# Performance work log

Hardware: AMD Instinct MI355X
Metric: run time of the kernel (lower is better)

## Reference

```python
import jax, jax.numpy as jnp
import numpy as np

D_MODEL = 2048
N_HEADS = 32
N_KV_HEADS = 8
ROPE_BASE = 10000.0


def setup_inputs() -> dict:
    key = jax.random.key(0)
    ks = jax.random.split(key, 5)
    b, s, d = 2, 2048, D_MODEL
    hd = d // N_HEADS
    scale = 0.02
    return {
        "x": jax.random.normal(ks[0], (b, s, d), jnp.float32),
        "wq": jax.random.normal(ks[1], (N_HEADS * hd, d), jnp.float32) * scale,
        "wk": jax.random.normal(ks[2], (N_KV_HEADS * hd, d), jnp.float32) * scale,
        "wv": jax.random.normal(ks[3], (N_KV_HEADS * hd, d), jnp.float32) * scale,
        "wo": jax.random.normal(ks[4], (d, N_HEADS * hd), jnp.float32) * scale,
    }


def _rope_cos_sin(seq_len, head_dim):
    # theta_j = base^(-2j/d); freqs[i, j] = i * theta_j; repeat-interleave x2 on last dim
    theta = 1.0 / (ROPE_BASE ** (jnp.arange(0, head_dim, 2, dtype=jnp.float32) / head_dim))
    freqs = jnp.arange(seq_len, dtype=jnp.float32)[:, None] * theta[None, :]  # [S, hd/2]
    cos = jnp.repeat(jnp.cos(freqs), 2, axis=-1)[None, :, None, :]  # [1, S, 1, hd]
    sin = jnp.repeat(jnp.sin(freqs), 2, axis=-1)[None, :, None, :]
    return cos, sin


def _rotate(t):
    # interleaved rotate-half: (x0, x1, x2, x3, ...) -> (-x1, x0, -x3, x2, ...)
    t1 = t[..., ::2]
    t2 = t[..., 1::2]
    return jnp.stack([-t2, t1], axis=-1).reshape(t.shape)


def reference(x, wq, wk, wv, wo):
    b, s, d = x.shape
    hd = d // N_HEADS
    n_rep = N_HEADS // N_KV_HEADS

    q = (x @ wq.T).reshape(b, s, N_HEADS, hd)       # [b, s, H, hd]
    k = (x @ wk.T).reshape(b, s, N_KV_HEADS, hd)    # [b, s, G, hd]
    v = (x @ wv.T).reshape(b, s, N_KV_HEADS, hd)

    cos, sin = _rope_cos_sin(s, hd)
    q = q * cos + _rotate(q) * sin
    k = k * cos + _rotate(k) * sin

    # GQA without physical KV replication: group query heads by shared KV head.
    # repeat_interleave(n_rep, dim=2) maps kv head g -> query heads [g*n_rep, (g+1)*n_rep)
    qg = q.reshape(b, s, N_KV_HEADS, n_rep, hd)
    scale = 1.0 / jnp.sqrt(jnp.asarray(hd, q.dtype))
    scores = jnp.einsum('bqgrd,bkgd->bgrqk', qg, k) * scale  # [b, G, rep, Sq, Sk]

    causal = jnp.tril(jnp.ones((s, s), dtype=bool))
    scores = jnp.where(causal[None, None, None], scores, jnp.asarray(-jnp.inf, scores.dtype))
    attn = jax.nn.softmax(scores, axis=-1)

    out = jnp.einsum('bgrqk,bkgd->bqgrd', attn, v).reshape(b, s, N_HEADS * hd)
    return out @ wo.T
```

## Files before the change

### kernel.cpp

```cpp
#include <hip/hip_runtime.h>

typedef unsigned short u16;
typedef __attribute__((ext_vector_type(8))) short bf16x8;
typedef __attribute__((ext_vector_type(4))) float f32x4;

#define LOG2E 1.44269504088896340736f

__device__ inline u16 f2b(float f) {
    unsigned int u = __builtin_bit_cast(unsigned int, f);
    unsigned int r = u + 0x7fffu + ((u >> 16) & 1u);
    return (u16)(r >> 16);
}
__device__ inline float b2f(u16 h) {
    unsigned int u = ((unsigned int)h) << 16;
    return __builtin_bit_cast(float, u);
}

#define GLOAD_LDS16(g, l) \
    __builtin_amdgcn_global_load_lds( \
        (const __attribute__((address_space(1))) unsigned int*)(g), \
        (__attribute__((address_space(3))) unsigned int*)(l), 16, 0, 0)

__global__ __launch_bounds__(256) void cast_all(
    const float* __restrict__ x, const float* __restrict__ wq,
    const float* __restrict__ wk, const float* __restrict__ wv,
    const float* __restrict__ wo, u16* __restrict__ xb,
    u16* __restrict__ wqkvb, u16* __restrict__ wob) {
    long i = ((long)blockIdx.x * 256 + threadIdx.x) * 8;
    const float* s;
    u16* d;
    if (i < 8388608)       { s = x  + i;              d = xb + i; }
    else if (i < 12582912) { s = wq + (i - 8388608);  d = wqkvb + (i - 8388608); }
    else if (i < 13631488) { s = wk + (i - 12582912); d = wqkvb + 4194304 + (i - 12582912); }
    else if (i < 14680064) { s = wv + (i - 13631488); d = wqkvb + 5242880 + (i - 13631488); }
    else                   { s = wo + (i - 14680064); d = wob + (i - 14680064); }
    float4 v0 = *(const float4*)s;
    float4 v1 = *(const float4*)(s + 4);
    ushort4 o0 = make_ushort4(f2b(v0.x), f2b(v0.y), f2b(v0.z), f2b(v0.w));
    ushort4 o1 = make_ushort4(f2b(v1.x), f2b(v1.y), f2b(v1.z), f2b(v1.w));
    *(ushort4*)d = o0;
    *(ushort4*)(d + 4) = o1;
}

__global__ __launch_bounds__(256) void rope_vtrans(
    u16* __restrict__ qkv, u16* __restrict__ VT, float qscale) {
    const int S = 2048, RS = 3072;
    int tid = threadIdx.x;
    if (blockIdx.x < 5120) {
        int idx = blockIdx.x * 256 + tid;
        int row = idx / 320;
        int rem = idx - row * 320;
        int head = rem >> 3, chunk = rem & 7;
        int pos = row & 2047;
        int coloff;
        float scale;
        if (head < 32) { coloff = head * 64;               scale = qscale; }
        else           { coloff = 2048 + (head - 32) * 64; scale = 1.0f; }
        u16* p = qkv + (size_t)row * RS + coloff + chunk * 8;
        bf16x8 v = *(bf16x8*)p;
        float t0 = exp2f((float)(chunk * 4) * -0.41524101186092f);
        const float tc[4] = {1.0f, 0.74989420933246f, 0.56234132519035f, 0.42169650342858f};
        float fpos = (float)pos;
        #pragma unroll
        for (int i = 0; i < 4; i++) {
            float f = fpos * (t0 * tc[i]);
            float rev = f * 0.15915494309189535f;
            rev = rev - floorf(rev);
            float sn = __builtin_amdgcn_sinf(rev);
            float cs = __builtin_amdgcn_cosf(rev);
            float e0 = b2f((u16)v[2 * i]), e1 = b2f((u16)v[2 * i + 1]);
            v[2 * i]     = (short)f2b((e0 * cs - e1 * sn) * scale);
            v[2 * i + 1] = (short)f2b((e1 * cs + e0 * sn) * scale);
        }
        *(bf16x8*)p = v;
    } else {
        int bid = blockIdx.x - 5120;
        int st = bid & 31, g = (bid >> 5) & 7, b = bid >> 8;
        __shared__ u16 T[64 * 72];
        for (int c = tid; c < 512; c += 256) {
            int sr = c >> 3, dc = (c & 7) * 8;
            *(bf16x8*)&T[sr * 72 + dc] =
                *(const bf16x8*)(qkv + ((size_t)b * S + st * 64 + sr) * RS + 2560 + g * 64 + dc);
        }
        __syncthreads();
        for (int c = tid; c < 512; c += 256) {
            int d = c >> 3, sc = (c & 7) * 8;
            bf16x8 o;
            #pragma unroll
            for (int j = 0; j < 8; j++) o[j] = (short)T[(sc + j) * 72 + d];
            *(bf16x8*)(VT + ((size_t)((b * 8 + g) * 64 + d)) * S + st * 64 + sc) = o;
        }
    }
}

__global__ __launch_bounds__(256) void gemm_bt128(
    const u16* __restrict__ A, const u16* __restrict__ B, void* __restrict__ Cv,
    int M, int N, int K, int c_is_f32) {
    __shared__ u16 As[128 * 32];
    __shared__ u16 Bs[128 * 32];
    const int tid = threadIdx.x;
    const int lane = tid & 63, wave = tid >> 6;
    const int ln = lane & 15, quad = lane >> 4;
    const int wm = wave >> 1, wn = wave & 1;
    const int m0 = blockIdx.y * 128, n0 = blockIdx.x * 128;

    const int srow = wave * 16 + (lane >> 2);
    const int skc = (lane & 3) * 8;
    const u16* Ag = A + (size_t)(m0 + srow) * K + skc;
    const u16* Bg = B + (size_t)(n0 + srow) * K + skc;

    f32x4 acc[4][4] = {};
    for (int k0 = 0; k0 < K; k0 += 32) {
        #pragma unroll
        for (int t = 0; t < 2; t++) {
            GLOAD_LDS16(Ag + (size_t)t * 64 * K + k0, As + t * 2048 + wave * 512);
            GLOAD_LDS16(Bg + (size_t)t * 64 * K + k0, Bs + t * 2048 + wave * 512);
        }
        __syncthreads();

        bf16x8 af[4], bfr[4];
        #pragma unroll
        for (int i = 0; i < 4; i++) {
            af[i]  = *(const bf16x8*)&As[(wm * 64 + i * 16 + ln) * 32 + quad * 8];
            bfr[i] = *(const bf16x8*)&Bs[(wn * 64 + i * 16 + ln) * 32 + quad * 8];
        }
        #pragma unroll
        for (int mi = 0; mi < 4; mi++)
            #pragma unroll
            for (int nt = 0; nt < 4; nt++)
                acc[mi][nt] = __builtin_amdgcn_mfma_f32_16x16x32_bf16(
                    af[mi], bfr[nt], acc[mi][nt], 0, 0, 0);
        __syncthreads();
    }

    #pragma unroll
    for (int mi = 0; mi < 4; mi++)
        #pragma unroll
        for (int nt = 0; nt < 4; nt++)
            #pragma unroll
            for (int r = 0; r < 4; r++) {
                int row = m0 + wm * 64 + mi * 16 + quad * 4 + r;
                int col = n0 + wn * 64 + nt * 16 + ln;
                float v = acc[mi][nt][r];
                if (c_is_f32) ((float*)Cv)[(size_t)row * N + col] = v;
                else          ((u16*)Cv)[(size_t)row * N + col] = f2b(v);
            }
}

__global__ __launch_bounds__(256) void attn_kernel(
    const u16* __restrict__ QKV, const u16* __restrict__ VT, u16* __restrict__ O) {
    const int S = 2048, RS = 3072, DO = 2048;
    const int b = blockIdx.z, h = blockIdx.y, p = blockIdx.x;
    const int g = h >> 2;
    const int qtl = p, qth = (S / 64 - 1) - p;
    const int tid = threadIdx.x;
    const int lane = tid & 63, wave = tid >> 6;
    const int ln = lane & 15, quad = lane >> 4;

    __shared__ u16 Ks[64 * 72];
    __shared__ u16 Psh[64 * 68];
    __shared__ u16 Psl[64 * 68];

    const u16* Qb = QKV + (size_t)b * S * RS + h * 64 + quad * 8;
    bf16x8 aqh0 = *(const bf16x8*)(Qb + (size_t)(qth * 64 + wave * 16 + ln) * RS);
    bf16x8 aqh1 = *(const bf16x8*)(Qb + (size_t)(qth * 64 + wave * 16 + ln) * RS + 32);
    bf16x8 aql0 = *(const bf16x8*)(Qb + (size_t)(qtl * 64 + wave * 16 + ln) * RS);
    bf16x8 aql1 = *(const bf16x8*)(Qb + (size_t)(qtl * 64 + wave * 16 + ln) * RS + 32);

    const u16* Kb = QKV + (size_t)b * S * RS + 2048 + g * 64;
    const u16* VTb = VT + (size_t)(b * 8 + g) * 64 * S;

    const bf16x8 vones = {0x3F80, 0x3F80, 0x3F80, 0x3F80, 0x3F80, 0x3F80, 0x3F80, 0x3F80};

    f32x4 acch[5] = {}, accl[5] = {};

    const int r0 = tid >> 3;
    const int dc0 = (tid & 7) * 8;
    bf16x8 kreg0, kreg1;
    auto loadK = [&](int kt) {
        kreg0 = *(const bf16x8*)(Kb + (size_t)(kt * 64 + r0) * RS + dc0);
        kreg1 = *(const bf16x8*)(Kb + (size_t)(kt * 64 + r0 + 32) * RS + dc0);
    };

    auto body = [&](int kt, bool DUAL, bool MH, bool ML) {
        __syncthreads();
        *(bf16x8*)&Ks[r0 * 72 + dc0] = kreg0;
        *(bf16x8*)&Ks[(r0 + 32) * 72 + dc0] = kreg1;
        __syncthreads();
        if (kt < qth) loadK(kt + 1);

        bf16x8 vr[2][4];
        #pragma unroll
        for (int kk = 0; kk < 2; kk++)
            #pragma unroll
            for (int nt = 0; nt < 4; nt++)
                vr[kk][nt] = *(const bf16x8*)(VTb + (size_t)(nt * 16 + ln) * S
                                              + kt * 64 + kk * 32 + quad * 8);

        f32x4 sh[4] = {}, sl[4] = {};
        __builtin_amdgcn_s_setprio(1);
        #pragma unroll
        for (int nt = 0; nt < 4; nt++) {
            bf16x8 bk0 = *(const bf16x8*)&Ks[(nt * 16 + ln) * 72 + quad * 8];
            bf16x8 bk1 = *(const bf16x8*)&Ks[(nt * 16 + ln) * 72 + 32 + quad * 8];
            sh[nt] = __builtin_amdgcn_mfma_f32_16x16x32_bf16(aqh0, bk0, sh[nt], 0, 0, 0);
            sh[nt] = __builtin_amdgcn_mfma_f32_16x16x32_bf16(aqh1, bk1, sh[nt], 0, 0, 0);
            if (DUAL) {
                sl[nt] = __builtin_amdgcn_mfma_f32_16x16x32_bf16(aql0, bk0, sl[nt], 0, 0, 0);
                sl[nt] = __builtin_amdgcn_mfma_f32_16x16x32_bf16(aql1, bk1, sl[nt], 0, 0, 0);
            }
        }
        __builtin_amdgcn_s_setprio(0);

        if (MH) {
            #pragma unroll
            for (int nt = 0; nt < 4; nt++)
                #pragma unroll
                for (int r = 0; r < 4; r++)
                    if (nt * 16 + ln > wave * 16 + quad * 4 + r) sh[nt][r] = -INFINITY;
        }
        #pragma unroll
        for (int nt = 0; nt < 4; nt++)
            #pragma unroll
            for (int r = 0; r < 4; r++) {
                float pv = exp2f(sh[nt][r]);
                Psh[(wave * 16 + quad * 4 + r) * 68 + nt * 16 + ln] =
                    (u16)(__builtin_bit_cast(unsigned int, pv) >> 16);
            }
        if (DUAL) {
            if (ML) {
                #pragma unroll
                for (int nt = 0; nt < 4; nt++)
                    #pragma unroll
                    for (int r = 0; r < 4; r++)
                        if (nt * 16 + ln > wave * 16 + quad * 4 + r) sl[nt][r] = -INFINITY;
            }
            #pragma unroll
            for (int nt = 0; nt < 4; nt++)
                #pragma unroll
                for (int r = 0; r < 4; r++) {
                    float pv = exp2f(sl[nt][r]);
                    Psl[(wave * 16 + quad * 4 + r) * 68 + nt * 16 + ln] =
                        (u16)(__builtin_bit_cast(unsigned int, pv) >> 16);
                }
        }

        __builtin_amdgcn_s_setprio(1);
        #pragma unroll
        for (int kk = 0; kk < 2; kk++) {
            bf16x8 aph = *(const bf16x8*)&Psh[(wave * 16 + ln) * 68 + kk * 32 + quad * 8];
            #pragma unroll
            for (int nt = 0; nt < 4; nt++)
                acch[nt] = __builtin_amdgcn_mfma_f32_16x16x32_bf16(aph, vr[kk][nt], acch[nt], 0, 0, 0);
            acch[4] = __builtin_amdgcn_mfma_f32_16x16x32_bf16(aph, vones, acch[4], 0, 0, 0);
            if (DUAL) {
                bf16x8 apl = *(const bf16x8*)&Psl[(wave * 16 + ln) * 68 + kk * 32 + quad * 8];
                #pragma unroll
                for (int nt = 0; nt < 4; nt++)
                    accl[nt] = __builtin_amdgcn_mfma_f32_16x16x32_bf16(apl, vr[kk][nt], accl[nt], 0, 0, 0);
                accl[4] = __builtin_amdgcn_mfma_f32_16x16x32_bf16(apl, vones, accl[4], 0, 0, 0);
            }
        }
        __builtin_amdgcn_s_setprio(0);
    };

    loadK(0);
    for (int kt = 0; kt < qtl; kt++) body(kt, true, false, false);
    body(qtl, true, false, true);
    for (int kt = qtl + 1; kt < qth; kt++) body(kt, false, false, false);
    body(qth, false, true, false);

    u16* Ob = O + (size_t)b * S * DO + h * 64;
    #pragma unroll
    for (int r = 0; r < 4; r++) {
        float invh = 1.0f / acch[4][r];
        float invl = 1.0f / accl[4][r];
        int qh = qth * 64 + wave * 16 + quad * 4 + r;
        int ql = qtl * 64 + wave * 16 + quad * 4 + r;
        #pragma unroll
        for (int nt = 0; nt < 4; nt++) {
            Ob[(size_t)qh * DO + nt * 16 + ln] = f2b(acch[nt][r] * invh);
            Ob[(size_t)ql * DO + nt * 16 + ln] = f2b(accl[nt][r] * invl);
        }
    }
}

extern "C" void kernel_launch(void* const* d_in, const int* in_sizes, int n_in,
                              void* d_out, int out_size, void* d_ws, size_t ws_size,
                              hipStream_t stream) {
    const float* x  = (const float*)d_in[0];
    const float* wq = (const float*)d_in[1];
    const float* wk = (const float*)d_in[2];
    const float* wv = (const float*)d_in[3];
    const float* wo = (const float*)d_in[4];

    const int B = 2, S = 2048, D = 2048, H = 32, KVH = 8;
    const int M = B * S;
    const int NQKV = 3072;

    char* ws = (char*)d_ws;
    size_t off = 0;
    auto alloc = [&](size_t bytes) {
        void* p = ws + off;
        off += (bytes + 255) & ~(size_t)255;
        return p;
    };
    u16* xb    = (u16*)alloc((size_t)M * D * 2);
    u16* wqkvb = (u16*)alloc((size_t)NQKV * D * 2);
    u16* wob   = (u16*)alloc((size_t)D * D * 2);
    u16* QKV   = (u16*)alloc((size_t)M * NQKV * 2);
    u16* AO = xb;
    u16* VT = wqkvb;

    cast_all<<<dim3(9216), 256, 0, stream>>>(x, wq, wk, wv, wo, xb, wqkvb, wob);

    gemm_bt128<<<dim3(NQKV / 128, M / 128), 256, 0, stream>>>(xb, wqkvb, QKV, M, NQKV, D, 0);

    const float sscale = 0.125f * LOG2E;
    rope_vtrans<<<dim3(5632), 256, 0, stream>>>(QKV, VT, sscale);

    attn_kernel<<<dim3(S / 128, H, B), 256, 0, stream>>>(QKV, VT, AO);

    gemm_bt128<<<dim3(D / 128, M / 128), 256, 0, stream>>>(AO, wob, d_out, M, D, D, 1);
}
```

Baseline: 377.3 us.

## Double-buffer K tiles and prefetch V in attention; swizzle GEMM workgroups

Attention now keeps two LDS K tiles, loads K two tiles ahead and V one tile ahead in registers. This replaces the two barriers per iteration with a single one at the end of the body, so global load latency can overlap compute. The GEMM remaps workgroup IDs in chunks of eight, likely to improve L2 locality across XCDs. The cost is more LDS and more registers in attention, which could lower occupancy.

```diff
diff --git a/kernel.cpp b/kernel.cpp
--- a/kernel.cpp
+++ b/kernel.cpp
@@ -102,7 +102,13 @@
     const int lane = tid & 63, wave = tid >> 6;
     const int ln = lane & 15, quad = lane >> 4;
     const int wm = wave >> 1, wn = wave & 1;
-    const int m0 = blockIdx.y * 128, n0 = blockIdx.x * 128;
+
+    const int gx = gridDim.x;
+    const int nwg = gx * gridDim.y;
+    const int bid = blockIdx.y * gx + blockIdx.x;
+    const int cpx = nwg >> 3;
+    const int swz = (bid & 7) * cpx + (bid >> 3);
+    const int m0 = (swz / gx) * 128, n0 = (swz % gx) * 128;
 
     const int srow = wave * 16 + (lane >> 2);
     const int skc = (lane & 3) * 8;
@@ -157,7 +163,7 @@
     const int lane = tid & 63, wave = tid >> 6;
     const int ln = lane & 15, quad = lane >> 4;
 
-    __shared__ u16 Ks[64 * 72];
+    __shared__ u16 Ks[2][64 * 72];
     __shared__ u16 Psh[64 * 68];
     __shared__ u16 Psl[64 * 68];
 
@@ -177,32 +183,35 @@
     const int r0 = tid >> 3;
     const int dc0 = (tid & 7) * 8;
     bf16x8 kreg0, kreg1;
+    bf16x8 vr[2][4];
     auto loadK = [&](int kt) {
         kreg0 = *(const bf16x8*)(Kb + (size_t)(kt * 64 + r0) * RS + dc0);
         kreg1 = *(const bf16x8*)(Kb + (size_t)(kt * 64 + r0 + 32) * RS + dc0);
     };
-
-    auto body = [&](int kt, bool DUAL, bool MH, bool ML) {
-        __syncthreads();
-        *(bf16x8*)&Ks[r0 * 72 + dc0] = kreg0;
-        *(bf16x8*)&Ks[(r0 + 32) * 72 + dc0] = kreg1;
-        __syncthreads();
-        if (kt < qth) loadK(kt + 1);
-
-        bf16x8 vr[2][4];
+    auto loadV = [&](int kt) {
         #pragma unroll
         for (int kk = 0; kk < 2; kk++)
             #pragma unroll
             for (int nt = 0; nt < 4; nt++)
                 vr[kk][nt] = *(const bf16x8*)(VTb + (size_t)(nt * 16 + ln) * S
                                               + kt * 64 + kk * 32 + quad * 8);
+    };
+
+    auto body = [&](int kt, bool DUAL, bool MH, bool ML) {
+        u16* KsC = &Ks[kt & 1][0];
+        u16* KsN = &Ks[(kt & 1) ^ 1][0];
+        if (kt < qth) {
+            *(bf16x8*)&KsN[r0 * 72 + dc0] = kreg0;
+            *(bf16x8*)&KsN[(r0 + 32) * 72 + dc0] = kreg1;
+        }
+        if (kt + 2 <= qth) loadK(kt + 2);
 
         f32x4 sh[4] = {}, sl[4] = {};
         __builtin_amdgcn_s_setprio(1);
         #pragma unroll
         for (int nt = 0; nt < 4; nt++) {
-            bf16x8 bk0 = *(const bf16x8*)&Ks[(nt * 16 + ln) * 72 + quad * 8];
-            bf16x8 bk1 = *(const bf16x8*)&Ks[(nt * 16 + ln) * 72 + 32 + quad * 8];
+            bf16x8 bk0 = *(const bf16x8*)&KsC[(nt * 16 + ln) * 72 + quad * 8];
+            bf16x8 bk1 = *(const bf16x8*)&KsC[(nt * 16 + ln) * 72 + 32 + quad * 8];
             sh[nt] = __builtin_amdgcn_mfma_f32_16x16x32_bf16(aqh0, bk0, sh[nt], 0, 0, 0);
             sh[nt] = __builtin_amdgcn_mfma_f32_16x16x32_bf16(aqh1, bk1, sh[nt], 0, 0, 0);
             if (DUAL) {
@@ -262,9 +271,18 @@
             }
         }
         __builtin_amdgcn_s_setprio(0);
+
+        if (kt < qth) loadV(kt + 1);
+        __syncthreads();
     };
 
     loadK(0);
+    loadV(0);
+    *(bf16x8*)&Ks[0][r0 * 72 + dc0] = kreg0;
+    *(bf16x8*)&Ks[0][(r0 + 32) * 72 + dc0] = kreg1;
+    loadK(1);
+    __syncthreads();
+
     for (int kt = 0; kt < qtl; kt++) body(kt, true, false, false);
     body(qtl, true, false, true);
     for (int kt = qtl + 1; kt < qth; kt++) body(kt, false, false, false);
```

Result: no change. 375.9 us (-0.4%).
